# Performance work log

Hardware: AMD Instinct MI355X
Metric: run time of the kernel (lower is better)

## Reference

```python
import jax, jax.numpy as jnp
import numpy as np

N_NODES = 10000
N_EDGES = 160000
D = 128        # embedding_dim = in/out channels
E_DIM = 32     # edge feature dim
HEADS = 3
N_ETYPES = 64
ROUNDS = 2     # num_message_rounds
NEG_SLOPE = 0.2


def _lookup_maxnorm(table, idx):
    # torch Embedding(max_norm=1): rows with L2 norm > 1 are renormalized to norm 1
    v = table[idx]
    n = jnp.linalg.norm(v, axis=-1, keepdims=True)
    return v / jnp.maximum(n, 1.0)


def _edge_gat(x, src, dst, edge_attr, weight, att, euw, bias):
    # x: [N, D]; src/dst: [E] (self loops included); edge_attr: [E, E_DIM]
    N = x.shape[0]
    H = HEADS
    C = weight.shape[1] // H
    xh = (x @ weight).reshape(N, H, C)                 # [N, H, C]
    x_j = xh[src]                                      # gather source nodes  [E, H, C]
    x_i = xh[dst]                                      # gather target nodes  [E, H, C]
    ea = jnp.broadcast_to(edge_attr[:, None, :], (src.shape[0], H, edge_attr.shape[-1]))
    xj_cat = jnp.concatenate([x_j, ea], axis=-1)       # [E, H, C+E_DIM]
    # attention logits: (cat(x_i, x_j, e) * att).sum(-1)
    alpha = jnp.sum(jnp.concatenate([x_i, xj_cat], axis=-1) * att, axis=-1)  # [E, H]
    alpha = jax.nn.leaky_relu(alpha, NEG_SLOPE)
    # scatter-softmax over incoming edges of each dst node (stable)
    m = jax.ops.segment_max(alpha, dst, num_segments=N)        # [N, H]
    a = jnp.exp(alpha - m[dst])
    denom = jax.ops.segment_sum(a, dst, num_segments=N)        # [N, H]
    a = a / denom[dst]
    # weighted scatter-add aggregate
    aggr = jax.ops.segment_sum(xj_cat * a[..., None], dst, num_segments=N)  # [N, H, C+E_DIM]
    return aggr.mean(axis=1) @ euw + bias                       # [N, C]


def setup_inputs() -> dict:
    key = jax.random.key(0)
    ks = jax.random.split(key, 13)
    x_idx = jnp.arange(N_NODES, dtype=jnp.int32)
    src = jax.random.randint(ks[0], (N_EDGES,), 0, N_NODES, dtype=jnp.int32)
    off = jax.random.randint(ks[1], (N_EDGES,), 1, N_NODES, dtype=jnp.int32)
    dst = (src + off) % N_NODES    # guaranteed self-loop-free
    edge_index = jnp.stack([src, dst])
    edge_attr_idx = jax.random.randint(ks[2], (N_EDGES,), 0, N_ETYPES, dtype=jnp.int32)
    def g(k, shape):
        return jax.random.normal(k, shape, jnp.float32) * np.float32(np.sqrt(2.0 / sum(shape)))
    node_emb = g(ks[3], (N_NODES, D))
    edge_emb = g(ks[4], (N_ETYPES, E_DIM))
    w1 = g(ks[5], (D, HEADS * D))
    att1 = g(ks[6], (1, HEADS, 2 * D + E_DIM))
    euw1 = g(ks[7], (D + E_DIM, D))
    b1 = jnp.zeros((D,), jnp.float32)
    w2 = g(ks[8], (D, HEADS * D))
    att2 = g(ks[9], (1, HEADS, 2 * D + E_DIM))
    euw2 = g(ks[10], (D + E_DIM, D))
    b2 = jnp.zeros((D,), jnp.float32)
    return dict(x_idx=x_idx, edge_index=edge_index, edge_attr_idx=edge_attr_idx,
                node_emb=node_emb, edge_emb=edge_emb,
                w1=w1, att1=att1, euw1=euw1, b1=b1,
                w2=w2, att2=att2, euw2=euw2, b2=b2)


def reference(x_idx, edge_index, edge_attr_idx, node_emb, edge_emb,
              w1, att1, euw1, b1, w2, att2, euw2, b2):
    N = node_emb.shape[0]
    src0, dst0 = edge_index[0], edge_index[1]
    loop = jnp.arange(N, dtype=src0.dtype)
    src = jnp.concatenate([src0, loop])
    dst = jnp.concatenate([dst0, loop])
    x = _lookup_maxnorm(node_emb, x_idx)               # [N, D]
    ea = edge_emb[edge_attr_idx]                       # [E0, E_DIM]
    ea_full = jnp.concatenate([ea, jnp.zeros((N, ea.shape[-1]), ea.dtype)], axis=0)
    for _ in range(ROUNDS):
        # eval mode: dropout is identity
        x = jax.nn.elu(_edge_gat(x, src, dst, ea_full, w1, att1, euw1, b1))
        x = _edge_gat(x, src, dst, ea_full, w2, att2, euw2, b2)
    return x
```

## Files before the change

kernel.cpp:

```cpp
#include <hip/hip_runtime.h>
#include <hip/hip_bf16.h>

typedef __hip_bfloat16 bf16;
typedef __attribute__((ext_vector_type(8))) short short8;
typedef __attribute__((ext_vector_type(4))) float f32x4;

__device__ __forceinline__ float b2f(bf16 v) { return __bfloat162float(v); }
__device__ __forceinline__ float2 i2f2(int w) {
  float lo = __uint_as_float(((unsigned)w) << 16);
  float hi = __uint_as_float(((unsigned)w) & 0xFFFF0000u);
  return make_float2(lo, hi);
}
__device__ __forceinline__ unsigned f2bfb(float f) {
  unsigned u = __float_as_uint(f);
  unsigned r = 0x7FFFu + ((u >> 16) & 1u);
  return (u + r) >> 16;
}
__device__ __forceinline__ unsigned pk2(float a, float b) {
  return f2bfb(a) | (f2bfb(b) << 16);
}
__device__ __forceinline__ float ldv(const void* p, int i, int f) {
  return f ? ((const float*)p)[i] : b2f(((const bf16*)p)[i]);
}

__global__ __launch_bounds__(256) void wconv_kernel(
    const void* __restrict__ ee, const void* __restrict__ w1,
    const void* __restrict__ a1, const void* __restrict__ eu1,
    const void* __restrict__ b1, const void* __restrict__ w2,
    const void* __restrict__ a2, const void* __restrict__ eu2,
    const void* __restrict__ b2, int* __restrict__ flag,
    float* __restrict__ eef, float* __restrict__ att1f, float* __restrict__ att2f,
    float* __restrict__ b1f, float* __restrict__ b2f,
    bf16* __restrict__ WT1, bf16* __restrict__ WT2,
    bf16* __restrict__ euT1, bf16* __restrict__ euT2,
    float* __restrict__ s_et, int* __restrict__ counts, int N) {
  __shared__ int cnt;
  __shared__ int fl;
  if (threadIdx.x == 0) cnt = 0;
  __syncthreads();
  const unsigned short* probe = (const unsigned short*)w1;
  int local = 0;
#pragma unroll
  for (int k = 0; k < 8; ++k) {
    int e = (probe[threadIdx.x * 8 + k] >> 7) & 0xFF;
    if (e >= 160) local++;
  }
  if (local) atomicAdd(&cnt, local);
  __syncthreads();
  if (threadIdx.x == 0) {
    fl = (cnt > 16) ? 1 : 0;
    if (blockIdx.x == 0) *flag = fl;
  }
  __syncthreads();
  int f = fl;

  int i = blockIdx.x * 256 + threadIdx.x;
  if (i < 2048) {
    eef[i] = ldv(ee, i, f);
  } else if (i < 2912) {
    att1f[i - 2048] = ldv(a1, i - 2048, f);
  } else if (i < 3776) {
    att2f[i - 2912] = ldv(a2, i - 2912, f);
  } else if (i < 3904) {
    b1f[i - 3776] = ldv(b1, i - 3776, f);
  } else if (i < 4032) {
    b2f[i - 3904] = ldv(b2, i - 3904, f);
  } else if (i < 53184) {
    int j = i - 4032; int c = j >> 7, k = j & 127;
    WT1[j] = __float2bfloat16(ldv(w1, k * 384 + c, f));
  } else if (i < 102336) {
    int j = i - 53184; int c = j >> 7, k = j & 127;
    WT2[j] = __float2bfloat16(ldv(w2, k * 384 + c, f));
  } else if (i < 122816) {
    int j = i - 102336; int c = j / 160, k = j % 160;
    euT1[j] = __float2bfloat16(ldv(eu1, k * 128 + c, f));
  } else if (i < 143296) {
    int j = i - 122816; int c = j / 160, k = j % 160;
    euT2[j] = __float2bfloat16(ldv(eu2, k * 128 + c, f));
  } else if (i < 143296 + N) {
    counts[i - 143296] = 0;
  }

  if (blockIdx.x == 0) {
    for (int id = threadIdx.x; id < 2 * 65 * 3; id += 256) {
      int l = id / (65 * 3);
      int r = id % (65 * 3);
      int t = r / 3, h = r % 3;
      const void* att = l ? a2 : a1;
      float s = 0.0f;
      if (t < 64) {
        for (int d = 0; d < 32; ++d)
          s += ldv(ee, t * 32 + d, f) * ldv(att, h * 288 + 256 + d, f);
      }
      s_et[id] = s;
    }
  }
}

__global__ __launch_bounds__(256) void prep_kernel(
    const int* __restrict__ x_idx, const void* __restrict__ node_emb,
    const int* __restrict__ flag, bf16* __restrict__ xb,
    int* __restrict__ counts, const int* __restrict__ dst, int E0, int N) {
  int wid = threadIdx.x >> 6, lane = threadIdx.x & 63;
  int n = blockIdx.x * 4 + wid;
  if (n < N) {
    int idx = x_idx[n];
    if ((unsigned)idx >= (unsigned)N) idx = 0;
    float v0, v1;
    if (*flag) {
      const float* er = (const float*)node_emb + (size_t)idx * 128;
      v0 = er[lane]; v1 = er[lane + 64];
    } else {
      const bf16* er = (const bf16*)node_emb + (size_t)idx * 128;
      v0 = b2f(er[lane]); v1 = b2f(er[lane + 64]);
    }
    float ss = v0 * v0 + v1 * v1;
#pragma unroll
    for (int d = 32; d > 0; d >>= 1) ss += __shfl_xor(ss, d);
    float norm = sqrtf(ss);
    float scale = norm > 1.0f ? 1.0f / norm : 1.0f;
    xb[(size_t)n * 128 + lane] = __float2bfloat16(v0 * scale);
    xb[(size_t)n * 128 + 64 + lane] = __float2bfloat16(v1 * scale);
  }
  int gid = blockIdx.x * 256 + threadIdx.x;
  int stride = gridDim.x * 256;
  for (int i = gid; i < E0; i += stride) {
    int d = dst[i];
    if ((unsigned)d >= (unsigned)N) d = 0;
    atomicAdd(&counts[d], 1);
  }
}

__global__ __launch_bounds__(1024) void scan_kernel(
    int* __restrict__ counts, int* __restrict__ row_ptr, int N) {
  __shared__ int wsum[16];
  int t = threadIdx.x;
  int chunk = (N + 1023) >> 10;
  int lo = t * chunk;
  int hi = lo + chunk;
  if (lo > N) lo = N;
  if (hi > N) hi = N;
  int s = 0;
  for (int i = lo; i < hi; ++i) s += counts[i] + 1;
  int lane = t & 63, wv = t >> 6;
  int incl = s;
#pragma unroll
  for (int d = 1; d < 64; d <<= 1) {
    int u = __shfl_up(incl, d);
    if (lane >= d) incl += u;
  }
  if (lane == 63) wsum[wv] = incl;
  __syncthreads();
  if (t == 0) {
    int run = 0;
#pragma unroll
    for (int w = 0; w < 16; ++w) { int c = wsum[w]; wsum[w] = run; run += c; }
  }
  __syncthreads();
  int run = incl - s + wsum[wv];
  for (int i = lo; i < hi; ++i) {
    int c = counts[i] + 1;
    row_ptr[i] = run;
    counts[i] = run;
    run += c;
  }
  if (t == 1023) row_ptr[N] = run;
}

__global__ __launch_bounds__(256) void scatter_kernel(
    const int* __restrict__ src, const int* __restrict__ dst,
    const int* __restrict__ et, int* __restrict__ cursor,
    int* __restrict__ packed, int E0, int N) {
  int E = E0 + N;
  int i = blockIdx.x * blockDim.x + threadIdx.x;
  if (i < E0) {
    int d = dst[i];
    if ((unsigned)d >= (unsigned)N) d = 0;
    int p = atomicAdd(&cursor[d], 1);
    if ((unsigned)p >= (unsigned)E) p = 0;
    int t = et[i] & 63;
    packed[p] = (src[i] & 0xFFFF) | (t << 16);
  } else if (i < E) {
    int n = i - E0;
    int p = atomicAdd(&cursor[n], 1);
    if ((unsigned)p >= (unsigned)E) p = 0;
    packed[p] = (n & 0xFFFF) | (64 << 16);
  }
}

__global__ __launch_bounds__(384) void gemm_xh_s_mfma(
    const bf16* __restrict__ x, const bf16* __restrict__ WT,
    const float* __restrict__ attf, bf16* __restrict__ xh,
    float* __restrict__ s_i, float* __restrict__ s_j, int N) {
  __shared__ float lds_i[6][32];
  __shared__ float lds_j[6][32];
  int wave = threadIdx.x >> 6, lane = threadIdx.x & 63;
  int row_base = blockIdx.x * 32;
  int quad = lane >> 4, r16 = lane & 15;
  int rowA = row_base + r16;      if (rowA >= N) rowA = N - 1;
  int rowB = row_base + 16 + r16; if (rowB >= N) rowB = N - 1;
  const short8* apA = (const short8*)(x + (size_t)rowA * 128 + quad * 8);
  const short8* apB = (const short8*)(x + (size_t)rowB * 128 + quad * 8);
  short8 aA[4], aB[4];
#pragma unroll
  for (int kk = 0; kk < 4; ++kk) { aA[kk] = apA[kk * 4]; aB[kk] = apB[kk * 4]; }

  float piA[4] = {0.f, 0.f, 0.f, 0.f}, pjA[4] = {0.f, 0.f, 0.f, 0.f};
  float piB[4] = {0.f, 0.f, 0.f, 0.f}, pjB[4] = {0.f, 0.f, 0.f, 0.f};
#pragma unroll
  for (int j = 0; j < 4; ++j) {
    int col = wave * 64 + j * 16 + r16;
    const short8* bp = (const short8*)(WT + (size_t)col * 128 + quad * 8);
    short8 b[4];
#pragma unroll
    for (int kk = 0; kk < 4; ++kk) b[kk] = bp[kk * 4];
    f32x4 accA = {0.f, 0.f, 0.f, 0.f};
    f32x4 accB = {0.f, 0.f, 0.f, 0.f};
#pragma unroll
    for (int kk = 0; kk < 4; ++kk) {
      accA = __builtin_amdgcn_mfma_f32_16x16x32_bf16(aA[kk], b[kk], accA, 0, 0, 0);
      accB = __builtin_amdgcn_mfma_f32_16x16x32_bf16(aB[kk], b[kk], accB, 0, 0, 0);
    }
    int h = col >> 7, fi = col & 127, pair = fi >> 1, sub = fi & 1;
    size_t base = (size_t)pair * 6 + h * 2 + sub;
#pragma unroll
    for (int r = 0; r < 4; ++r) {
      int nA = row_base + quad * 4 + r;
      int nB = row_base + 16 + quad * 4 + r;
      if (nA < N) xh[(size_t)nA * 384 + base] = __float2bfloat16(accA[r]);
      if (nB < N) xh[(size_t)nB * 384 + base] = __float2bfloat16(accB[r]);
    }
    float ai = attf[h * 288 + fi];
    float aj = attf[h * 288 + 128 + fi];
#pragma unroll
    for (int r = 0; r < 4; ++r) {
      piA[r] = fmaf(accA[r], ai, piA[r]);
      pjA[r] = fmaf(accA[r], aj, pjA[r]);
      piB[r] = fmaf(accB[r], ai, piB[r]);
      pjB[r] = fmaf(accB[r], aj, pjB[r]);
    }
  }
#pragma unroll
  for (int d = 1; d < 16; d <<= 1) {
#pragma unroll
    for (int r = 0; r < 4; ++r) {
      piA[r] += __shfl_xor(piA[r], d);
      pjA[r] += __shfl_xor(pjA[r], d);
      piB[r] += __shfl_xor(piB[r], d);
      pjB[r] += __shfl_xor(pjB[r], d);
    }
  }
  if (r16 == 0) {
#pragma unroll
    for (int r = 0; r < 4; ++r) {
      lds_i[wave][quad * 4 + r] = piA[r];
      lds_j[wave][quad * 4 + r] = pjA[r];
      lds_i[wave][16 + quad * 4 + r] = piB[r];
      lds_j[wave][16 + quad * 4 + r] = pjB[r];
    }
  }
  __syncthreads();
  int m = threadIdx.x;
  if (m < 96) {
    int h = m / 32, r = m % 32;
    int node = row_base + r;
    if (node < N) s_i[node * 3 + h] = lds_i[2 * h][r] + lds_i[2 * h + 1][r];
  } else if (m < 192) {
    int tt = m - 96;
    int h = tt / 32, r = tt % 32;
    int node = row_base + r;
    if (node < N) s_j[node * 3 + h] = lds_j[2 * h][r] + lds_j[2 * h + 1][r];
  }
}

__global__ __launch_bounds__(256) void edge_aggr_kernel(
    const int* __restrict__ xh_i, const float* __restrict__ s_i,
    const float* __restrict__ s_j, const float* __restrict__ s_et,
    const float2* __restrict__ eef2, const int* __restrict__ row_ptr,
    const int* __restrict__ packed, unsigned* __restrict__ aggr_u,
    int N, int E) {
  __shared__ float lds[2][512];
  int wid = threadIdx.x >> 6, lane = threadIdx.x & 63;
  int nodeLocal = wid >> 1, w = wid & 1;
  int n0 = blockIdx.x * 2 + nodeLocal;
  int n = n0 < N ? n0 : N - 1;
  int start = row_ptr[n], end = row_ptr[n + 1];
  if (start < 0) start = 0;
  if (start > E) start = E;
  if (end < start) end = start;
  if (end > E) end = E;
  int deg = end - start;
  float si0 = s_i[n * 3 + 0], si1 = s_i[n * 3 + 1], si2 = s_i[n * 3 + 2];

  float p0r = 0.f, p1r = 0.f, p2r = 0.f;
  int pkr = 0;
  float dp0 = 0.0f, dp1 = 0.0f, dp2 = 0.0f;
  int slot = 2 * lane + w;
  if (slot < deg) {
    int p = packed[start + slot];
    int s = p & 0xFFFF; if (s >= N) s = N - 1;
    int t = (p >> 16) & 127; if (t > 64) t = 64;
    float a0 = si0 + s_j[s * 3 + 0] + s_et[t * 3 + 0];
    float a1 = si1 + s_j[s * 3 + 1] + s_et[t * 3 + 1];
    float a2 = si2 + s_j[s * 3 + 2] + s_et[t * 3 + 2];
    a0 = a0 > 0.0f ? a0 : 0.2f * a0;
    a1 = a1 > 0.0f ? a1 : 0.2f * a1;
    a2 = a2 > 0.0f ? a2 : 0.2f * a2;
    a0 = fminf(fmaxf(a0, -60.0f), 60.0f);
    a1 = fminf(fmaxf(a1, -60.0f), 60.0f);
    a2 = fminf(fmaxf(a2, -60.0f), 60.0f);
    p0r = __expf(a0); p1r = __expf(a1); p2r = __expf(a2);
    dp0 = p0r; dp1 = p1r; dp2 = p2r;
    pkr = s | (t << 16);
  }
#pragma unroll
  for (int d = 32; d > 0; d >>= 1) {
    dp0 += __shfl_xor(dp0, d);
    dp1 += __shfl_xor(dp1, d);
    dp2 += __shfl_xor(dp2, d);
  }
  float d0 = dp0, d1 = dp1, d2 = dp2;

  float2 ax0 = make_float2(0.f, 0.f), ax1 = ax0, ax2 = ax0;
  float2 ae0 = ax0, ae1 = ax0, ae2 = ax0;
  int capped = deg < 128 ? deg : 128;
  int cnt = (capped > w) ? ((capped - w + 1) >> 1) : 0;

  {
    int j = 0;
    for (; j + 2 <= cnt; j += 2) {
      int pkA = __shfl(pkr, j), pkB = __shfl(pkr, j + 1);
      float qA0 = __shfl(p0r, j), qB0 = __shfl(p0r, j + 1);
      float qA1 = __shfl(p1r, j), qB1 = __shfl(p1r, j + 1);
      float qA2 = __shfl(p2r, j), qB2 = __shfl(p2r, j + 1);
      int sA = pkA & 0xFFFF, tA = pkA >> 16;
      int sB = pkB & 0xFFFF, tB = pkB >> 16;
      const int* xpA = xh_i + (size_t)sA * 192 + lane * 3;
      const int* xpB = xh_i + (size_t)sB * 192 + lane * 3;
      int wA0 = xpA[0], wA1 = xpA[1], wA2 = xpA[2];
      int wB0 = xpB[0], wB1 = xpB[1], wB2 = xpB[2];
      float2 vA0 = i2f2(wA0), vA1 = i2f2(wA1), vA2 = i2f2(wA2);
      float2 vB0 = i2f2(wB0), vB1 = i2f2(wB1), vB2 = i2f2(wB2);
      ax0.x = fmaf(qA0, vA0.x, ax0.x); ax0.y = fmaf(qA0, vA0.y, ax0.y);
      ax1.x = fmaf(qA1, vA1.x, ax1.x); ax1.y = fmaf(qA1, vA1.y, ax1.y);
      ax2.x = fmaf(qA2, vA2.x, ax2.x); ax2.y = fmaf(qA2, vA2.y, ax2.y);
      ax0.x = fmaf(qB0, vB0.x, ax0.x); ax0.y = fmaf(qB0, vB0.y, ax0.y);
      ax1.x = fmaf(qB1, vB1.x, ax1.x); ax1.y = fmaf(qB1, vB1.y, ax1.y);
      ax2.x = fmaf(qB2, vB2.x, ax2.x); ax2.y = fmaf(qB2, vB2.y, ax2.y);
      if (lane < 16) {
        if (tA != 64) {
          float2 ev = eef2[tA * 16 + lane];
          ae0.x = fmaf(qA0, ev.x, ae0.x); ae0.y = fmaf(qA0, ev.y, ae0.y);
          ae1.x = fmaf(qA1, ev.x, ae1.x); ae1.y = fmaf(qA1, ev.y, ae1.y);
          ae2.x = fmaf(qA2, ev.x, ae2.x); ae2.y = fmaf(qA2, ev.y, ae2.y);
        }
        if (tB != 64) {
          float2 ev = eef2[tB * 16 + lane];
          ae0.x = fmaf(qB0, ev.x, ae0.x); ae0.y = fmaf(qB0, ev.y, ae0.y);
          ae1.x = fmaf(qB1, ev.x, ae1.x); ae1.y = fmaf(qB1, ev.y, ae1.y);
          ae2.x = fmaf(qB2, ev.x, ae2.x); ae2.y = fmaf(qB2, ev.y, ae2.y);
        }
      }
    }
    if (j < cnt) {
      int pkA = __shfl(pkr, j);
      float qA0 = __shfl(p0r, j), qA1 = __shfl(p1r, j), qA2 = __shfl(p2r, j);
      int sA = pkA & 0xFFFF, tA = pkA >> 16;
      const int* xpA = xh_i + (size_t)sA * 192 + lane * 3;
      int wA0 = xpA[0], wA1 = xpA[1], wA2 = xpA[2];
      float2 vA0 = i2f2(wA0), vA1 = i2f2(wA1), vA2 = i2f2(wA2);
      ax0.x = fmaf(qA0, vA0.x, ax0.x); ax0.y = fmaf(qA0, vA0.y, ax0.y);
      ax1.x = fmaf(qA1, vA1.x, ax1.x); ax1.y = fmaf(qA1, vA1.y, ax1.y);
      ax2.x = fmaf(qA2, vA2.x, ax2.x); ax2.y = fmaf(qA2, vA2.y, ax2.y);
      if (lane < 16 && tA != 64) {
        float2 ev = eef2[tA * 16 + lane];
        ae0.x = fmaf(qA0, ev.x, ae0.x); ae0.y = fmaf(qA0, ev.y, ae0.y);
        ae1.x = fmaf(qA1, ev.x, ae1.x); ae1.y = fmaf(qA1, ev.y, ae1.y);
        ae2.x = fmaf(qA2, ev.x, ae2.x); ae2.y = fmaf(qA2, ev.y, ae2.y);
      }
    }
  }

  if (w == 0) {
    for (int e = start + 128; e < end; ++e) {
      int p = packed[e];
      int s = p & 0xFFFF; if (s >= N) s = N - 1;
      int t = (p >> 16) & 127; if (t > 64) t = 64;
      float a0 = si0 + s_j[s * 3 + 0] + s_et[t * 3 + 0];
      float a1 = si1 + s_j[s * 3 + 1] + s_et[t * 3 + 1];
      float a2 = si2 + s_j[s * 3 + 2] + s_et[t * 3 + 2];
      a0 = a0 > 0.0f ? a0 : 0.2f * a0;
      a1 = a1 > 0.0f ? a1 : 0.2f * a1;
      a2 = a2 > 0.0f ? a2 : 0.2f * a2;
      a0 = fminf(fmaxf(a0, -60.0f), 60.0f);
      a1 = fminf(fmaxf(a1, -60.0f), 60.0f);
      a2 = fminf(fmaxf(a2, -60.0f), 60.0f);
      float p0 = __expf(a0), p1 = __expf(a1), p2 = __expf(a2);
      d0 += p0; d1 += p1; d2 += p2;
      const int* xp = xh_i + (size_t)s * 192 + lane * 3;
      float2 v0 = i2f2(xp[0]), v1 = i2f2(xp[1]), v2 = i2f2(xp[2]);
      ax0.x = fmaf(p0, v0.x, ax0.x); ax0.y = fmaf(p0, v0.y, ax0.y);
      ax1.x = fmaf(p1, v1.x, ax1.x); ax1.y = fmaf(p1, v1.y, ax1.y);
      ax2.x = fmaf(p2, v2.x, ax2.x); ax2.y = fmaf(p2, v2.y, ax2.y);
      if (t != 64 && lane < 16) {
        float2 ev = eef2[t * 16 + lane];
        ae0.x = fmaf(p0, ev.x, ae0.x); ae0.y = fmaf(p0, ev.y, ae0.y);
        ae1.x = fmaf(p1, ev.x, ae1.x); ae1.y = fmaf(p1, ev.y, ae1.y);
        ae2.x = fmaf(p2, ev.x, ae2.x); ae2.y = fmaf(p2, ev.y, ae2.y);
      }
    }
  }

  float* L = lds[nodeLocal];
  if (w == 1) {
    L[lane * 2 + 0] = ax0.x;       L[lane * 2 + 1] = ax0.y;
    L[128 + lane * 2 + 0] = ax1.x; L[128 + lane * 2 + 1] = ax1.y;
    L[256 + lane * 2 + 0] = ax2.x; L[256 + lane * 2 + 1] = ax2.y;
    if (lane < 16) {
      L[384 + lane * 2 + 0] = ae0.x; L[384 + lane * 2 + 1] = ae0.y;
      L[416 + lane * 2 + 0] = ae1.x; L[416 + lane * 2 + 1] = ae1.y;
      L[448 + lane * 2 + 0] = ae2.x; L[448 + lane * 2 + 1] = ae2.y;
    }
    if (lane == 0) { L[480] = d0; L[481] = d1; L[482] = d2; }
  }
  __syncthreads();
  if (w == 0 && n0 < N) {
    ax0.x += L[lane * 2 + 0];       ax0.y += L[lane * 2 + 1];
    ax1.x += L[128 + lane * 2 + 0]; ax1.y += L[128 + lane * 2 + 1];
    ax2.x += L[256 + lane * 2 + 0]; ax2.y += L[256 + lane * 2 + 1];
    if (lane < 16) {
      ae0.x += L[384 + lane * 2 + 0]; ae0.y += L[384 + lane * 2 + 1];
      ae1.x += L[416 + lane * 2 + 0]; ae1.y += L[416 + lane * 2 + 1];
      ae2.x += L[448 + lane * 2 + 0]; ae2.y += L[448 + lane * 2 + 1];
    }
    d0 += L[480]; d1 += L[481]; d2 += L[482];
    const float third = 1.0f / 3.0f;
    float i0 = third / fmaxf(d0, 1e-30f);
    float i1 = third / fmaxf(d1, 1e-30f);
    float i2 = third / fmaxf(d2, 1e-30f);
    aggr_u[(size_t)n0 * 80 + lane] =
        pk2(ax0.x * i0 + ax1.x * i1 + ax2.x * i2,
            ax0.y * i0 + ax1.y * i1 + ax2.y * i2);
    if (lane < 16)
      aggr_u[(size_t)n0 * 80 + 64 + lane] =
          pk2(ae0.x * i0 + ae1.x * i1 + ae2.x * i2,
              ae0.y * i0 + ae1.y * i1 + ae2.y * i2);
  }
}

__global__ __launch_bounds__(256) void gemm_out_mfma(
    const bf16* __restrict__ aggr, const bf16* __restrict__ euwT,
    const float* __restrict__ biasf, bf16* __restrict__ xb,
    void* __restrict__ dout, const int* __restrict__ flag,
    int N, int do_elu, int do_final) {
  int wave = threadIdx.x >> 6, lane = threadIdx.x & 63;
  int row_base = blockIdx.x * 16;
  int col_base = blockIdx.y * 64 + wave * 16;
  int quad = lane >> 4, r16 = lane & 15;
  int row = row_base + r16; if (row >= N) row = N - 1;
  int col = col_base + r16;
  f32x4 acc = {0.f, 0.f, 0.f, 0.f};
  const short8* ap = (const short8*)(aggr + (size_t)row * 160 + quad * 8);
  const short8* bp = (const short8*)(euwT + (size_t)col * 160 + quad * 8);
#pragma unroll
  for (int kk = 0; kk < 5; ++kk) {
    short8 a = ap[kk * 4];
    short8 b = bp[kk * 4];
    acc = __builtin_amdgcn_mfma_f32_16x16x32_bf16(a, b, acc, 0, 0, 0);
  }
  float bv = biasf[col];
  int f = *flag;
#pragma unroll
  for (int r = 0; r < 4; ++r) {
    int node = row_base + quad * 4 + r;
    if (node < N) {
      float v = acc[r] + bv;
      if (do_elu) v = v > 0.0f ? v : expm1f(v);
      if (do_final) {
        if (f) ((float*)dout)[(size_t)node * 128 + col] = v;
        else   ((bf16*)dout)[(size_t)node * 128 + col] = __float2bfloat16(v);
      } else {
        xb[(size_t)node * 128 + col] = __float2bfloat16(v);
      }
    }
  }
}

extern "C" void kernel_launch(void* const* d_in, const int* in_sizes, int n_in,
                              void* d_out, int out_size, void* d_ws, size_t ws_size,
                              hipStream_t stream) {
  const int* x_idx = (const int*)d_in[0];
  const int* edge_index = (const int*)d_in[1];
  const int* edge_attr_idx = (const int*)d_in[2];

  int N = in_sizes[0];
  int E0 = in_sizes[1] / 2;
  int E = E0 + N;
  const int* src = edge_index;
  const int* dst = edge_index + E0;

  size_t off = 0;
  char* base = (char*)d_ws;
  auto carve = [&](size_t bytes) -> void* {
    void* p = base + off;
    off += (bytes + 255) & ~(size_t)255;
    return p;
  };
  int* flag     = (int*)carve(256);
  int* counts   = (int*)carve((size_t)N * 4);
  int* row_ptr  = (int*)carve((size_t)(N + 1) * 4);
  int* packed   = (int*)carve((size_t)E * 4);
  float* s_i    = (float*)carve((size_t)N * 3 * 4);
  float* s_j    = (float*)carve((size_t)N * 3 * 4);
  float* s_et   = (float*)carve(2 * 65 * 3 * 4);
  float* eef    = (float*)carve(2048 * 4);
  float* att1f  = (float*)carve(864 * 4);
  float* att2f  = (float*)carve(864 * 4);
  float* b1f    = (float*)carve(128 * 4);
  float* b2f_   = (float*)carve(128 * 4);
  bf16* WT1     = (bf16*)carve(49152 * 2);
  bf16* WT2     = (bf16*)carve(49152 * 2);
  bf16* euT1    = (bf16*)carve(20480 * 2);
  bf16* euT2    = (bf16*)carve(20480 * 2);
  bf16* xh      = (bf16*)carve((size_t)N * 384 * 2 + 64);
  bf16* aggr    = (bf16*)carve((size_t)N * 160 * 2);
  bf16* xb      = (bf16*)d_out;
  (void)n_in; (void)out_size; (void)ws_size;

  wconv_kernel<<<(143296 + N + 255) / 256, 256, 0, stream>>>(
      d_in[4], d_in[5], d_in[6], d_in[7], d_in[8], d_in[9], d_in[10], d_in[11],
      d_in[12], flag, eef, att1f, att2f, b1f, b2f_, WT1, WT2, euT1, euT2,
      s_et, counts, N);
  int nb4 = (N + 3) / 4;
  prep_kernel<<<nb4, 256, 0, stream>>>(x_idx, d_in[3], flag, xb, counts, dst,
                                       E0, N);
  scan_kernel<<<1, 1024, 0, stream>>>(counts, row_ptr, N);
  scatter_kernel<<<(E + 255) / 256, 256, 0, stream>>>(src, dst, edge_attr_idx,
                                                      counts, packed, E0, N);

  const bf16* WTs[2] = {WT1, WT2};
  const float* atts[2] = {att1f, att2f};
  const bf16* euTs[2] = {euT1, euT2};
  const float* bs[2] = {b1f, b2f_};

  int nrb16 = (N + 15) / 16;
  int nrb32 = (N + 31) / 32;
  int nb2 = (N + 1) / 2;
  for (int round = 0; round < 2; ++round) {
    for (int l = 0; l < 2; ++l) {
      int do_elu = (l == 0) ? 1 : 0;
      int do_final = (round == 1 && l == 1) ? 1 : 0;
      gemm_xh_s_mfma<<<nrb32, 384, 0, stream>>>(xb, WTs[l], atts[l], xh,
                                                s_i, s_j, N);
      edge_aggr_kernel<<<nb2, 256, 0, stream>>>(
          (const int*)xh, s_i, s_j, s_et + l * 195, (const float2*)eef,
          row_ptr, packed, (unsigned*)aggr, N, E);
      gemm_out_mfma<<<dim3(nrb16, 2), 256, 0, stream>>>(
          aggr, euTs[l], bs[l], xb, d_out, flag, N, do_elu, do_final);
    }
  }
}
```

Baseline: 325.5 us.

## Fuse output GEMM with next layer's projection GEMM and attention scores

Adds a fused kernel that computes the per-layer output projection (aggr @ euw + bias, optional ELU) into a shared-memory tile, then immediately applies the next layer's weight GEMM and attention-score reductions. This removes the intermediate global write and read of x, and three kernel launches across the four layers. The fused kernel uses 16-row tiles with 384 threads, so each block performs more serial work, and the first two waves handle two output column tiles each, which gives uneven load across waves.

```diff
diff --git a/kernel.cpp b/kernel.cpp
--- a/kernel.cpp
+++ b/kernel.cpp
@@ -268,6 +268,100 @@
   } else if (m < 192) {
     int tt = m - 96;
     int h = tt / 32, r = tt % 32;
+    int node = row_base + r;
+    if (node < N) s_j[node * 3 + h] = lds_j[2 * h][r] + lds_j[2 * h + 1][r];
+  }
+}
+
+__global__ __launch_bounds__(384) void fox_kernel(
+    const bf16* __restrict__ aggr, const bf16* __restrict__ euwT,
+    const float* __restrict__ biasf, int do_elu,
+    const bf16* __restrict__ WT, const float* __restrict__ attf,
+    bf16* __restrict__ xh, float* __restrict__ s_i, float* __restrict__ s_j,
+    int N) {
+  __shared__ bf16 xtile[16][136];
+  __shared__ float lds_i[6][16];
+  __shared__ float lds_j[6][16];
+  int wave = threadIdx.x >> 6, lane = threadIdx.x & 63;
+  int quad = lane >> 4, r16 = lane & 15;
+  int row_base = blockIdx.x * 16;
+  int row = row_base + r16; if (row >= N) row = N - 1;
+
+  const short8* ap = (const short8*)(aggr + (size_t)row * 160 + quad * 8);
+  short8 aa[5];
+#pragma unroll
+  for (int kk = 0; kk < 5; ++kk) aa[kk] = ap[kk * 4];
+  for (int t = wave; t < 8; t += 6) {
+    int col = t * 16 + r16;
+    const short8* bp = (const short8*)(euwT + (size_t)col * 160 + quad * 8);
+    f32x4 acc = {0.f, 0.f, 0.f, 0.f};
+#pragma unroll
+    for (int kk = 0; kk < 5; ++kk)
+      acc = __builtin_amdgcn_mfma_f32_16x16x32_bf16(aa[kk], bp[kk * 4], acc, 0, 0, 0);
+    float bv = biasf[col];
+#pragma unroll
+    for (int r = 0; r < 4; ++r) {
+      float v = acc[r] + bv;
+      if (do_elu) v = v > 0.0f ? v : expm1f(v);
+      xtile[quad * 4 + r][col] = __float2bfloat16(v);
+    }
+  }
+  __syncthreads();
+
+  short8 a[4];
+#pragma unroll
+  for (int kk = 0; kk < 4; ++kk)
+    a[kk] = *(const short8*)(&xtile[r16][quad * 8 + kk * 32]);
+
+  float pi_r[4] = {0.f, 0.f, 0.f, 0.f};
+  float pj_r[4] = {0.f, 0.f, 0.f, 0.f};
+#pragma unroll
+  for (int j = 0; j < 4; ++j) {
+    int col = wave * 64 + j * 16 + r16;
+    const short8* bp = (const short8*)(WT + (size_t)col * 128 + quad * 8);
+    f32x4 acc = {0.f, 0.f, 0.f, 0.f};
+#pragma unroll
+    for (int kk = 0; kk < 4; ++kk)
+      acc = __builtin_amdgcn_mfma_f32_16x16x32_bf16(a[kk], bp[kk * 4], acc, 0, 0, 0);
+    int h = col >> 7, fi = col & 127, pair = fi >> 1, sub = fi & 1;
+    size_t base = (size_t)pair * 6 + h * 2 + sub;
+#pragma unroll
+    for (int r = 0; r < 4; ++r) {
+      int node = row_base + quad * 4 + r;
+      if (node < N) xh[(size_t)node * 384 + base] = __float2bfloat16(acc[r]);
+    }
+    float ai = attf[h * 288 + fi];
+    float aj = attf[h * 288 + 128 + fi];
+#pragma unroll
+    for (int r = 0; r < 4; ++r) {
+      pi_r[r] = fmaf(acc[r], ai, pi_r[r]);
+      pj_r[r] = fmaf(acc[r], aj, pj_r[r]);
+    }
+  }
+#pragma unroll
+  for (int d = 1; d < 16; d <<= 1) {
+#pragma unroll
+    for (int r = 0; r < 4; ++r) {
+      pi_r[r] += __shfl_xor(pi_r[r], d);
+      pj_r[r] += __shfl_xor(pj_r[r], d);
+    }
+  }
+  if (r16 == 0) {
+#pragma unroll
+    for (int r = 0; r < 4; ++r) {
+      lds_i[wave][quad * 4 + r] = pi_r[r];
+      lds_j[wave][quad * 4 + r] = pj_r[r];
+    }
+  }
+  __syncthreads();
+  int m = threadIdx.x;
+  if (m < 48) {
+    int h = m / 16, r = m % 16;
+    int node = row_base + r;
+    if (node < N) s_i[node * 3 + h] = lds_i[2 * h][r] + lds_i[2 * h + 1][r];
+  } else if (m < 96) {
+    int tt = m - 48;
+    int h = tt / 16, r = tt % 16;
     int node = row_base + r;
     if (node < N) s_j[node * 3 + h] = lds_j[2 * h][r] + lds_j[2 * h + 1][r];
   }
@@ -450,9 +544,8 @@
 
 __global__ __launch_bounds__(256) void gemm_out_mfma(
     const bf16* __restrict__ aggr, const bf16* __restrict__ euwT,
-    const float* __restrict__ biasf, bf16* __restrict__ xb,
-    void* __restrict__ dout, const int* __restrict__ flag,
-    int N, int do_elu, int do_final) {
+    const float* __restrict__ biasf, void* __restrict__ dout,
+    const int* __restrict__ flag, int N) {
   int wave = threadIdx.x >> 6, lane = threadIdx.x & 63;
   int row_base = blockIdx.x * 16;
   int col_base = blockIdx.y * 64 + wave * 16;
@@ -475,13 +568,8 @@
     int node = row_base + quad * 4 + r;
     if (node < N) {
       float v = acc[r] + bv;
-      if (do_elu) v = v > 0.0f ? v : expm1f(v);
-      if (do_final) {
-        if (f) ((float*)dout)[(size_t)node * 128 + col] = v;
-        else   ((bf16*)dout)[(size_t)node * 128 + col] = __float2bfloat16(v);
-      } else {
-        xb[(size_t)node * 128 + col] = __float2bfloat16(v);
-      }
+      if (f) ((float*)dout)[(size_t)node * 128 + col] = v;
+      else   ((bf16*)dout)[(size_t)node * 128 + col] = __float2bfloat16(v);
     }
   }
 }
@@ -538,25 +626,29 @@
   scatter_kernel<<<(E + 255) / 256, 256, 0, stream>>>(src, dst, edge_attr_idx,
                                                       counts, packed, E0, N);
 
-  const bf16* WTs[2] = {WT1, WT2};
-  const float* atts[2] = {att1f, att2f};
-  const bf16* euTs[2] = {euT1, euT2};
-  const float* bs[2] = {b1f, b2f_};
-
   int nrb16 = (N + 15) / 16;
   int nrb32 = (N + 31) / 32;
   int nb2 = (N + 1) / 2;
-  for (int round = 0; round < 2; ++round) {
-    for (int l = 0; l < 2; ++l) {
-      int do_elu = (l == 0) ? 1 : 0;
-      int do_final = (round == 1 && l == 1) ? 1 : 0;
-      gemm_xh_s_mfma<<<nrb32, 384, 0, stream>>>(xb, WTs[l], atts[l], xh,
-                                                s_i, s_j, N);
-      edge_aggr_kernel<<<nb2, 256, 0, stream>>>(
-          (const int*)xh, s_i, s_j, s_et + l * 195, (const float2*)eef,
-          row_ptr, packed, (unsigned*)aggr, N, E);
-      gemm_out_mfma<<<dim3(nrb16, 2), 256, 0, stream>>>(
-          aggr, euTs[l], bs[l], xb, d_out, flag, N, do_elu, do_final);
-    }
-  }
-}
+
+  gemm_xh_s_mfma<<<nrb32, 384, 0, stream>>>(xb, WT1, att1f, xh, s_i, s_j, N);
+  edge_aggr_kernel<<<nb2, 256, 0, stream>>>(
+      (const int*)xh, s_i, s_j, s_et, (const float2*)eef,
+      row_ptr, packed, (unsigned*)aggr, N, E);
+  fox_kernel<<<nrb16, 384, 0, stream>>>(aggr, euT1, b1f, 1, WT2, att2f,
+                                        xh, s_i, s_j, N);
+  edge_aggr_kernel<<<nb2, 256, 0, stream>>>(
+      (const int*)xh, s_i, s_j, s_et + 195, (const float2*)eef,
+      row_ptr, packed, (unsigned*)aggr, N, E);
+  fox_kernel<<<nrb16, 384, 0, stream>>>(aggr, euT2, b2f_, 0, WT1, att1f,
+                                        xh, s_i, s_j, N);
+  edge_aggr_kernel<<<nb2, 256, 0, stream>>>(
+      (const int*)xh, s_i, s_j, s_et, (const float2*)eef,
+      row_ptr, packed, (unsigned*)aggr, N, E);
+  fox_kernel<<<nrb16, 384, 0, stream>>>(aggr, euT1, b1f, 1, WT2, att2f,
+                                        xh, s_i, s_j, N);
+  edge_aggr_kernel<<<nb2, 256, 0, stream>>>(
+      (const int*)xh, s_i, s_j, s_et + 195, (const float2*)eef,
+      row_ptr, packed, (unsigned*)aggr, N, E);
+  gemm_out_mfma<<<dim3(nrb16, 2), 256, 0, stream>>>(aggr, euT2, b2f_,
+                                                    d_out, flag, N);
+}
```

Measured after the change: 318.0 us. 2.3% less time.
